# Kernel optimization log

Hardware: AMD Instinct MI355X
Metric: run time of the kernel (lower is better)

The kernel has to match this reference:

```python
import jax, jax.numpy as jnp
import numpy as np

VOCAB = 100
EMB = 256
HID = 256
B = 8
S = 2048


def setup_inputs() -> dict:
    key = jax.random.key(0)
    ks = jax.random.split(key, 12)
    s_e = 1.0 / np.sqrt(EMB)
    s_h = 1.0 / np.sqrt(HID)
    return {
        "x": jax.random.randint(ks[0], (B, S), 0, VOCAB),
        "embedding": jax.random.normal(ks[1], (VOCAB, EMB), jnp.float32),
        "w_ih": jax.random.uniform(ks[2], (3 * HID, EMB), jnp.float32, -s_e, s_e),
        "w_hh": jax.random.uniform(ks[3], (3 * HID, HID), jnp.float32, -s_h, s_h),
        "b_ih": jax.random.uniform(ks[4], (3 * HID,), jnp.float32, -s_h, s_h),
        "b_hh": jax.random.uniform(ks[5], (3 * HID,), jnp.float32, -s_h, s_h),
        "attn_w": jax.random.uniform(ks[6], (HID, HID), jnp.float32, -s_h, s_h),
        "attn_b": jax.random.uniform(ks[7], (HID,), jnp.float32, -s_h, s_h),
        "comb_w": jax.random.uniform(ks[8], (HID, 2 * HID), jnp.float32, -s_h, s_h),
        "comb_b": jax.random.uniform(ks[9], (HID,), jnp.float32, -s_h, s_h),
        "fc_w": jax.random.uniform(ks[10], (VOCAB, HID), jnp.float32, -s_h, s_h),
        "fc_b": jax.random.uniform(ks[11], (VOCAB,), jnp.float32, -s_h, s_h),
    }


def _gru(emb, w_ih, w_hh, b_ih, b_hh):
    # emb: [B, S, E]; PyTorch GRU gate order: r, z, n
    xg = jnp.einsum('bse,ge->bsg', emb, w_ih) + b_ih  # [B, S, 3H]
    h0 = jnp.zeros((emb.shape[0], HID), emb.dtype)

    def step(h, xg_t):
        hg = h @ w_hh.T + b_hh
        xr, xz, xn = jnp.split(xg_t, 3, axis=-1)
        hr, hz, hn = jnp.split(hg, 3, axis=-1)
        r = jax.nn.sigmoid(xr + hr)
        z = jax.nn.sigmoid(xz + hz)
        n = jnp.tanh(xn + r * hn)
        h_new = (1.0 - z) * n + z * h
        return h_new, h_new

    h_last, hs = jax.lax.scan(step, h0, jnp.swapaxes(xg, 0, 1))
    return jnp.swapaxes(hs, 0, 1), h_last  # [B,S,H], [B,H]


def reference(x, embedding, w_ih, w_hh, b_ih, b_hh, attn_w, attn_b, comb_w, comb_b, fc_w, fc_b):
    emb = embedding[x]  # [B, S, E]
    all_h, h_last = _gru(emb, w_ih, w_hh, b_ih, b_hh)
    keys = jnp.einsum('bsh,kh->bsk', all_h, attn_w) + attn_b  # [B,S,H]
    scores = jnp.einsum('bqh,bkh->bqk', all_h, keys)  # [B,S,S]
    seq = all_h.shape[1]
    causal = jnp.tril(jnp.ones((seq, seq), bool))
    scores = jnp.where(causal[None], scores, -jnp.inf)
    attn = jax.nn.softmax(scores, axis=-1)
    context = jnp.einsum('bqk,bkh->bqh', attn, all_h)  # [B,S,H]
    combined = jnp.concatenate([all_h, context], axis=-1)
    combined = jnp.tanh(jnp.einsum('bsd,hd->bsh', combined, comb_w) + comb_b)
    output = jnp.einsum('bsh,vh->bsv', combined, fc_w) + fc_b
    return output, h_last[None]  # hidden: [num_layers=1, B, H]
```

## Files before the change

kernel.cpp:

```cpp
#include <hip/hip_runtime.h>

#define SEQ  2048
#define NB   8
#define HD   256
#define G3   768
#define NV   100
#define KVB  32

typedef float f32x4 __attribute__((ext_vector_type(4)));
typedef int   i32x4 __attribute__((ext_vector_type(4)));
typedef short s16x8 __attribute__((ext_vector_type(8)));
typedef unsigned short u16x4 __attribute__((ext_vector_type(4)));

#define INV26 1.490116119384765625e-8f

__device__ __forceinline__ float rcp_fast(float x) {
  return __builtin_amdgcn_rcpf(x);
}
__device__ __forceinline__ float sigm(float x) {
  x = fminf(fmaxf(x, -30.f), 30.f);
  return rcp_fast(1.f + __expf(-x));
}
__device__ __forceinline__ float tanh_fast(float x) {
  x = fminf(fmaxf(x, -15.f), 15.f);
  float e = __expf(2.f * x);
  return (e - 1.f) * rcp_fast(e + 1.f);
}
__device__ __forceinline__ void cvt_hilo(float f, unsigned short& h, unsigned short& l) {
  unsigned u = __float_as_uint(f);
  h = (unsigned short)(u >> 16);
  float r = f - __uint_as_float(u & 0xffff0000u);
  l = (unsigned short)(__float_as_uint(r) >> 16);
}

__global__ __launch_bounds__(256) void build_table(
    const float* __restrict__ emb, const float* __restrict__ w_ih,
    const float* __restrict__ b_ih, float* __restrict__ table) {
  __shared__ float eL[256];
  __shared__ float wL[256][37];
  int v = blockIdx.x, tid = threadIdx.x;
  eL[tid] = emb[v * HD + tid];
  for (int gt = 0; gt < 3; ++gt) {
    float acc = b_ih[gt * 256 + tid];
    for (int e0 = 0; e0 < HD; e0 += 32) {
      __syncthreads();
      #pragma unroll
      for (int i = 0; i < 32; ++i) {
        int idx = tid + i * 256;
        int r = idx >> 5, c = idx & 31;
        wL[r][c] = w_ih[(size_t)(gt * 256 + r) * HD + e0 + c];
      }
      __syncthreads();
      #pragma unroll
      for (int c = 0; c < 32; ++c) acc += eL[e0 + c] * wL[tid][c];
    }
    table[((size_t)v * 256 + tid) * 4 + gt] = acc;
  }
}

__global__ void __launch_bounds__(512) gru_scan(
    const int* __restrict__ x, const float* __restrict__ w_hh,
    const float* __restrict__ b_hh, const float* __restrict__ table,
    float* __restrict__ all_h, float* __restrict__ h_last) {
  __shared__ __align__(16) signed char hpk[2][2 * 272];
  __shared__ int xs[SEQ];
  const int b = blockIdx.x;
  int tid = threadIdx.x;
  int lane = tid & 63, wv = tid >> 6;
  int ncol = lane & 15, quad = lane >> 4;
  int usel = quad & 1;
  int j = wv * 32 + usel * 16 + ncol;

  for (int i = tid; i < SEQ; i += 512) xs[i] = x[b * SEQ + i];
  for (int i = tid; i < 2 * 272; i += 512)
    hpk[0][i] = (i >= 272) ? (signed char)-128 : 0;

  i32x4 bw[2][3][4];
  float Cn2[2][3];
  #pragma unroll
  for (int u = 0; u < 2; ++u) {
    #pragma unroll
    for (int t3 = 0; t3 < 3; ++t3) {
      int row = t3 * 256 + wv * 32 + u * 16 + ncol;
      int sw = 0;
      #pragma unroll
      for (int c = 0; c < 4; ++c) {
        const float* p = w_hh + (size_t)row * HD + c * 64 + quad * 16;
        unsigned pw[4] = {0u, 0u, 0u, 0u};
        #pragma unroll
        for (int e = 0; e < 16; ++e) {
          int q = __float2int_rn(p[e] * 2048.f);
          q = max(-127, min(127, q));
          sw += q;
          pw[e >> 2] |= ((unsigned)(q & 255)) << ((e & 3) * 8);
        }
        bw[u][t3][c] = (i32x4){(int)pw[0], (int)pw[1], (int)pw[2], (int)pw[3]};
      }
      sw += __shfl_xor(sw, 16);
      sw += __shfl_xor(sw, 32);
      Cn2[u][t3] = b_hh[row] + 128.f * (float)sw * INV26;
    }
  }
  float Csel[3];
  #pragma unroll
  for (int t3 = 0; t3 < 3; ++t3) Csel[t3] = usel ? Cn2[1][t3] : Cn2[0][t3];

  float hreg = 0.f, hpend = 0.f;
  __syncthreads();
  float xr, xz, xn;
  {
    int v = xs[0];
    f32x4 xg = *(const f32x4*)&table[((size_t)v * 256 + j) * 4];
    xr = xg[0]; xz = xg[1]; xn = xg[2];
  }
  int a_base = (ncol & 1) * 272 + quad * 16;

  for (int t = 0; t < SEQ; ++t) {
    const signed char* cb = hpk[t & 1];
    i32x4 a[4];
    #pragma unroll
    for (int c = 0; c < 4; ++c)
      a[c] = *(const i32x4*)&cb[a_base + c * 64];
    if (t > 0 && quad < 2)
      all_h[((size_t)b * SEQ + (t - 1)) * HD + j] = hpend;
    int vnext = xs[(t + 1 < SEQ) ? t + 1 : t];
    f32x4 xgn = *(const f32x4*)&table[((size_t)vnext * 256 + j) * 4];
    float hg[3];
    #pragma unroll
    for (int t3 = 0; t3 < 3; ++t3) {
      i32x4 A0 = {0, 0, 0, 0}, A1 = {0, 0, 0, 0};
      #pragma unroll
      for (int c = 0; c < 4; ++c) {
        A0 = __builtin_amdgcn_mfma_i32_16x16x64_i8(a[c], bw[0][t3][c], A0, 0, 0, 0);
        A1 = __builtin_amdgcn_mfma_i32_16x16x64_i8(a[c], bw[1][t3][c], A1, 0, 0, 0);
      }
      int d0 = usel ? A1[0] : A0[0];
      int d1 = usel ? A1[1] : A0[1];
      hg[t3] = ((float)d0 * 256.f + (float)d1) * INV26 + Csel[t3];
    }
    float r = sigm(xr + hg[0]);
    float z = sigm(xz + hg[1]);
    float n = tanh_fast(xn + r * hg[2]);
    float h = (1.f - z) * n + z * hreg;
    hreg = h;
    hpend = h;
    int q = min(__float2int_rn(h * 32768.f), 32767);
    int lou = q & 255;
    int hi8 = (q - lou) >> 8;
    signed char* nx = hpk[(t + 1) & 1];
    if (quad < 2) {
      nx[j] = (signed char)hi8;
      nx[272 + j] = (signed char)(lou - 128);
    }
    xr = xgn[0]; xz = xgn[1]; xn = xgn[2];
    __syncthreads();
  }
  if (quad < 2) {
    all_h[((size_t)b * SEQ + (SEQ - 1)) * HD + j] = hpend;
    h_last[b * HD + j] = hreg;
  }
}

template<int ACT>
__global__ __launch_bounds__(256) void gemm_bias(
    const float* __restrict__ A, int lda,
    const float* __restrict__ W, const float* __restrict__ bias,
    float* __restrict__ C, int ldc, int N, int K) {
  __shared__ float As[128][36];
  __shared__ float Ws[64][36];
  int tid = threadIdx.x;
  int m0 = blockIdx.y * 128, n0 = blockIdx.x * 64;
  int ml = tid & 31, g = tid >> 5;
  float acc[4][8];
  #pragma unroll
  for (int i = 0; i < 4; ++i)
    #pragma unroll
    for (int jj = 0; jj < 8; ++jj) acc[i][jj] = 0.f;
  for (int k0 = 0; k0 < K; k0 += 32) {
    __syncthreads();
    #pragma unroll
    for (int i = 0; i < 4; ++i) {
      int idx = tid + i * 256;
      int r = idx >> 3, c4 = (idx & 7) * 4;
      *(f32x4*)&As[r][c4] = *(const f32x4*)&A[(size_t)(m0 + r) * lda + k0 + c4];
    }
    #pragma unroll
    for (int i = 0; i < 2; ++i) {
      int idx = tid + i * 256;
      int r = idx >> 3, c4 = (idx & 7) * 4;
      f32x4 wv = {0.f, 0.f, 0.f, 0.f};
      if (n0 + r < N) wv = *(const f32x4*)&W[(size_t)(n0 + r) * K + k0 + c4];
      *(f32x4*)&Ws[r][c4] = wv;
    }
    __syncthreads();
    #pragma unroll
    for (int k4 = 0; k4 < 32; k4 += 4) {
      f32x4 av[4], wv8[8];
      #pragma unroll
      for (int i = 0; i < 4; ++i) av[i] = *(const f32x4*)&As[ml + i * 32][k4];
      #pragma unroll
      for (int jj = 0; jj < 8; ++jj) wv8[jj] = *(const f32x4*)&Ws[g * 8 + jj][k4];
      #pragma unroll
      for (int kk = 0; kk < 4; ++kk)
        #pragma unroll
        for (int i = 0; i < 4; ++i)
          #pragma unroll
          for (int jj = 0; jj < 8; ++jj)
            acc[i][jj] += av[i][kk] * wv8[jj][kk];
    }
  }
  #pragma unroll
  for (int i = 0; i < 4; ++i) {
    int m = m0 + ml + i * 32;
    #pragma unroll
    for (int jj = 0; jj < 8; ++jj) {
      int n = n0 + g * 8 + jj;
      if (n < N) {
        float val = acc[i][jj] + bias[n];
        if (ACT) val = tanh_fast(val);
        C[(size_t)m * ldc + n] = val;
      }
    }
  }
}

__global__ __launch_bounds__(256) void gemm_bias_cat(
    const float* __restrict__ A1, const float* __restrict__ A2,
    const float* __restrict__ W, const float* __restrict__ bias,
    float* __restrict__ C) {
  __shared__ float As[128][36];
  __shared__ float Ws[64][36];
  const int K = 512;
  int tid = threadIdx.x;
  int m0 = blockIdx.y * 128, n0 = blockIdx.x * 64;
  int ml = tid & 31, g = tid >> 5;
  float acc[4][8];
  #pragma unroll
  for (int i = 0; i < 4; ++i)
    #pragma unroll
    for (int jj = 0; jj < 8; ++jj) acc[i][jj] = 0.f;
  for (int k0 = 0; k0 < K; k0 += 32) {
    const float* src = (k0 < 256) ? A1 : A2;
    int kb = (k0 < 256) ? k0 : k0 - 256;
    __syncthreads();
    #pragma unroll
    for (int i = 0; i < 4; ++i) {
      int idx = tid + i * 256;
      int r = idx >> 3, c4 = (idx & 7) * 4;
      *(f32x4*)&As[r][c4] = *(const f32x4*)&src[(size_t)(m0 + r) * 256 + kb + c4];
    }
    #pragma unroll
    for (int i = 0; i < 2; ++i) {
      int idx = tid + i * 256;
      int r = idx >> 3, c4 = (idx & 7) * 4;
      *(f32x4*)&Ws[r][c4] = *(const f32x4*)&W[(size_t)(n0 + r) * K + k0 + c4];
    }
    __syncthreads();
    #pragma unroll
    for (int k4 = 0; k4 < 32; k4 += 4) {
      f32x4 av[4], wv8[8];
      #pragma unroll
      for (int i = 0; i < 4; ++i) av[i] = *(const f32x4*)&As[ml + i * 32][k4];
      #pragma unroll
      for (int jj = 0; jj < 8; ++jj) wv8[jj] = *(const f32x4*)&Ws[g * 8 + jj][k4];
      #pragma unroll
      for (int kk = 0; kk < 4; ++kk)
        #pragma unroll
        for (int i = 0; i < 4; ++i)
          #pragma unroll
          for (int jj = 0; jj < 8; ++jj)
            acc[i][jj] += av[i][kk] * wv8[jj][kk];
    }
  }
  #pragma unroll
  for (int i = 0; i < 4; ++i) {
    int m = m0 + ml + i * 32;
    #pragma unroll
    for (int jj = 0; jj < 8; ++jj) {
      int n = n0 + g * 8 + jj;
      C[(size_t)m * 256 + n] = tanh_fast(acc[i][jj] + bias[n]);
    }
  }
}

__global__ __launch_bounds__(256, 1) void attention_kernel(
    const float* __restrict__ all_h, const float* __restrict__ keys,
    float* __restrict__ ctxg) {
  __shared__ __align__(16) unsigned short KH[2][8][4][140], KL[2][8][4][140];
  __shared__ __align__(16) unsigned short VH[16][524], VL[16][524];
  __shared__ __align__(16) unsigned short PB[4][2][520];
  const int b = blockIdx.y, qb = blockIdx.x;
  int tid = threadIdx.x, lane = tid & 63, wv = tid >> 6;
  int lm = lane & 15, kg = lane >> 4;
  const float* hb = all_h + (size_t)b * SEQ * HD;
  const float* kb = keys  + (size_t)b * SEQ * HD;
  const int q0 = qb * 64 + wv * 16;

  s16x8 Qh[8], Ql[8];
  {
    const float* qp = hb + (size_t)(q0 + lm) * HD;
    #pragma unroll
    for (int ch = 0; ch < 8; ++ch) {
      union { s16x8 v; unsigned short u[8]; } uh, ul;
      f32x4 a0 = *(const f32x4*)&qp[ch * 32 + kg * 8];
      f32x4 a1 = *(const f32x4*)&qp[ch * 32 + kg * 8 + 4];
      #pragma unroll
      for (int e = 0; e < 4; ++e) {
        cvt_hilo(a0[e], uh.u[e], ul.u[e]);
        cvt_hilo(a1[e], uh.u[4 + e], ul.u[4 + e]);
      }
      Qh[ch] = uh.v; Ql[ch] = ul.v;
    }
  }

  f32x4 co[16];
  #pragma unroll
  for (int ht = 0; ht < 16; ++ht) co[ht] = (f32x4){0.f, 0.f, 0.f, 0.f};
  float mo[4] = {-3e38f, -3e38f, -3e38f, -3e38f};
  float lr[4] = {0.f, 0.f, 0.f, 0.f};

  const int nkt = 2 * qb + 2;
  f32x4 kreg[8], vreg[8];
  {
    #pragma unroll
    for (int i = 0; i < 8; ++i) {
      int idx = tid + i * 256;
      int r = idx >> 6, c = idx & 63;
      kreg[i] = *(const f32x4*)&kb[(size_t)r * HD + c * 4];
      vreg[i] = *(const f32x4*)&hb[(size_t)r * HD + c * 4];
    }
  }
  for (int kt = 0; kt < nkt; ++kt) {
    __syncthreads();
    #pragma unroll
    for (int i = 0; i < 8; ++i) {
      int idx = tid + i * 256;
      int r = idx >> 6, c = idx & 63;
      f32x4 kv = kreg[i];
      f32x4 vv = vreg[i];
      u16x4 khv, klv;
      #pragma unroll
      for (int e = 0; e < 4; ++e) {
        unsigned short h16, l16;
        cvt_hilo(kv[e], h16, l16);
        khv[e] = h16; klv[e] = l16;
      }
      int off = (r & 15) * 8 + (c & 1) * 4;
      *(u16x4*)&KH[r >> 4][c >> 3][(c & 7) >> 1][off] = khv;
      *(u16x4*)&KL[r >> 4][c >> 3][(c & 7) >> 1][off] = klv;
      int kgv = r >> 3, ev = r & 7, ht = c >> 2;
      #pragma unroll
      for (int e = 0; e < 4; ++e) {
        unsigned short h16, l16;
        cvt_hilo(vv[e], h16, l16);
        int o = (kgv * 16 + (c & 3) * 4 + e) * 8 + ev;
        VH[ht][o] = h16; VL[ht][o] = l16;
      }
    }
    __syncthreads();
    if (kt + 1 < nkt) {
      int k1 = (kt + 1) * KVB;
      #pragma unroll
      for (int i = 0; i < 8; ++i) {
        int idx = tid + i * 256;
        int r = idx >> 6, c = idx & 63;
        kreg[i] = *(const f32x4*)&kb[(size_t)(k1 + r) * HD + c * 4];
        vreg[i] = *(const f32x4*)&hb[(size_t)(k1 + r) * HD + c * 4];
      }
    }
    int k0 = kt * KVB;

    float s[4][2];
    #pragma unroll
    for (int g = 0; g < 2; ++g) {
      f32x4 a0 = {0.f,0.f,0.f,0.f}, a1 = {0.f,0.f,0.f,0.f}, a2 = {0.f,0.f,0.f,0.f};
      #pragma unroll
      for (int ch = 0; ch < 8; ++ch) {
        s16x8 bh = *(const s16x8*)&KH[g][ch][kg][lm * 8];
        s16x8 bl = *(const s16x8*)&KL[g][ch][kg][lm * 8];
        a0 = __builtin_amdgcn_mfma_f32_16x16x32_bf16(Qh[ch], bh, a0, 0, 0, 0);
        a1 = __builtin_amdgcn_mfma_f32_16x16x32_bf16(Ql[ch], bh, a1, 0, 0, 0);
        a2 = __builtin_amdgcn_mfma_f32_16x16x32_bf16(Qh[ch], bl, a2, 0, 0, 0);
      }
      #pragma unroll
      for (int r = 0; r < 4; ++r) s[r][g] = a0[r] + a1[r] + a2[r];
    }
    float p[4][2], al[4];
    #pragma unroll
    for (int r = 0; r < 4; ++r) {
      int qrow = q0 + kg * 4 + r;
      int va = (k0 + lm) <= qrow, vb = (k0 + 16 + lm) <= qrow;
      float ta = va ? s[r][0] : -3e38f;
      float tb = vb ? s[r][1] : -3e38f;
      float t = fmaxf(ta, tb);
      t = fmaxf(t, __shfl_xor(t, 1));
      t = fmaxf(t, __shfl_xor(t, 2));
      t = fmaxf(t, __shfl_xor(t, 4));
      t = fmaxf(t, __shfl_xor(t, 8));
      float mn = fmaxf(mo[r], t);
      al[r] = __expf(mo[r] - mn);
      float pa = va ? __expf(s[r][0] - mn) : 0.f;
      float pb = vb ? __expf(s[r][1] - mn) : 0.f;
      p[r][0] = pa; p[r][1] = pb;
      float rs = pa + pb;
      rs += __shfl_xor(rs, 1);
      rs += __shfl_xor(rs, 2);
      rs += __shfl_xor(rs, 4);
      rs += __shfl_xor(rs, 8);
      lr[r] = lr[r] * al[r] + rs;
      mo[r] = mn;
    }
    #pragma unroll
    for (int r = 0; r < 4; ++r)
      #pragma unroll
      for (int g = 0; g < 2; ++g) {
        unsigned short ph, pl;
        cvt_hilo(p[r][g], ph, pl);
        int key = g * 16 + lm;
        int o = ((key >> 3) * 16 + kg * 4 + r) * 8 + (key & 7);
        PB[wv][0][o] = ph;
        PB[wv][1][o] = pl;
      }
    s16x8 pah = *(const s16x8*)&PB[wv][0][lane * 8];
    s16x8 pal = *(const s16x8*)&PB[wv][1][lane * 8];
    #pragma unroll
    for (int ht = 0; ht < 16; ++ht) {
      f32x4 c = co[ht];
      #pragma unroll
      for (int r = 0; r < 4; ++r) c[r] *= al[r];
      s16x8 vh = *(const s16x8*)&VH[ht][lane * 8];
      s16x8 vl = *(const s16x8*)&VL[ht][lane * 8];
      c = __builtin_amdgcn_mfma_f32_16x16x32_bf16(pah, vh, c, 0, 0, 0);
      c = __builtin_amdgcn_mfma_f32_16x16x32_bf16(pah, vl, c, 0, 0, 0);
      c = __builtin_amdgcn_mfma_f32_16x16x32_bf16(pal, vh, c, 0, 0, 0);
      co[ht] = c;
    }
  }
  float li[4];
  #pragma unroll
  for (int r = 0; r < 4; ++r) li[r] = rcp_fast(lr[r]);
  #pragma unroll
  for (int ht = 0; ht < 16; ++ht)
    #pragma unroll
    for (int r = 0; r < 4; ++r)
      ctxg[((size_t)b * SEQ + q0 + kg * 4 + r) * HD + ht * 16 + lm] = co[ht][r] * li[r];
}

extern "C" void kernel_launch(void* const* d_in, const int* in_sizes, int n_in,
                              void* d_out, int out_size, void* d_ws, size_t ws_size,
                              hipStream_t stream) {
  (void)in_sizes; (void)n_in; (void)out_size; (void)ws_size;
  const int*   x      = (const int*)  d_in[0];
  const float* emb    = (const float*)d_in[1];
  const float* w_ih   = (const float*)d_in[2];
  const float* w_hh   = (const float*)d_in[3];
  const float* b_ih   = (const float*)d_in[4];
  const float* b_hh   = (const float*)d_in[5];
  const float* attn_w = (const float*)d_in[6];
  const float* attn_b = (const float*)d_in[7];
  const float* comb_w = (const float*)d_in[8];
  const float* comb_b = (const float*)d_in[9];
  const float* fc_w   = (const float*)d_in[10];
  const float* fc_b   = (const float*)d_in[11];
  float* out = (float*)d_out;

  float* ws    = (float*)d_ws;
  float* table = ws;
  float* all_h = table + 102400;
  float* keys  = all_h + 4194304;
  float* ctx   = keys  + 4194304;
  float* hlast = out + (size_t)NB * SEQ * NV;

  build_table<<<100, 256, 0, stream>>>(emb, w_ih, b_ih, table);
  gru_scan<<<NB, 512, 0, stream>>>(x, w_hh, b_hh, table, all_h, hlast);
  gemm_bias<0><<<dim3(4, 128), 256, 0, stream>>>(all_h, 256, attn_w, attn_b, keys, 256, 256, 256);
  attention_kernel<<<dim3(32, 8), 256, 0, stream>>>(all_h, keys, ctx);
  gemm_bias_cat<<<dim3(4, 128), 256, 0, stream>>>(all_h, ctx, comb_w, comb_b, keys);
  gemm_bias<0><<<dim3(2, 128), 256, 0, stream>>>(keys, 256, fc_w, fc_b, out, 100, 100, 256);
}
```

Before: 2.104 ms.

## Prepack attention keys as bf16 hi/lo in MFMA layout inside keys GEMM

```diff
diff --git a/kernel.cpp b/kernel.cpp
--- a/kernel.cpp
+++ b/kernel.cpp
@@ -105,7 +105,7 @@
   #pragma unroll
   for (int t3 = 0; t3 < 3; ++t3) Csel[t3] = usel ? Cn2[1][t3] : Cn2[0][t3];
 
-  float hreg = 0.f, hpend = 0.f;
+  float hreg = 0.f;
   __syncthreads();
   float xr, xz, xn;
   {
@@ -121,10 +121,6 @@
     #pragma unroll
     for (int c = 0; c < 4; ++c)
       a[c] = *(const i32x4*)&cb[a_base + c * 64];
-    if (t > 0 && quad < 2)
-      all_h[((size_t)b * SEQ + (t - 1)) * HD + j] = hpend;
-    int vnext = xs[(t + 1 < SEQ) ? t + 1 : t];
-    f32x4 xgn = *(const f32x4*)&table[((size_t)vnext * 256 + j) * 4];
     float hg[3];
     #pragma unroll
     for (int t3 = 0; t3 < 3; ++t3) {
@@ -143,7 +139,6 @@
     float n = tanh_fast(xn + r * hg[2]);
     float h = (1.f - z) * n + z * hreg;
     hreg = h;
-    hpend = h;
     int q = min(__float2int_rn(h * 32768.f), 32767);
     int lou = q & 255;
     int hi8 = (q - lou) >> 8;
@@ -151,14 +146,14 @@
     if (quad < 2) {
       nx[j] = (signed char)hi8;
       nx[272 + j] = (signed char)(lou - 128);
-    }
-    xr = xgn[0]; xz = xgn[1]; xn = xgn[2];
-    __syncthreads();
-  }
-  if (quad < 2) {
-    all_h[((size_t)b * SEQ + (SEQ - 1)) * HD + j] = hpend;
-    h_last[b * HD + j] = hreg;
-  }
+      all_h[((size_t)b * SEQ + t) * HD + j] = h;
+    }
+    int v = xs[(t + 1 < SEQ) ? t + 1 : t];
+    f32x4 xg = *(const f32x4*)&table[((size_t)v * 256 + j) * 4];
+    xr = xg[0]; xz = xg[1]; xn = xg[2];
+    __syncthreads();
+  }
+  if (quad < 2) h_last[b * HD + j] = hreg;
 }
 
 template<int ACT>
@@ -224,6 +219,72 @@
   }
 }
 
+__global__ __launch_bounds__(256) void gemm_keys_pack(
+    const float* __restrict__ A,
+    const float* __restrict__ W, const float* __restrict__ bias,
+    unsigned short* __restrict__ KP) {
+  __shared__ float As[128][36];
+  __shared__ float Ws[64][36];
+  const int K = 256;
+  int tid = threadIdx.x;
+  int m0 = blockIdx.y * 128, n0 = blockIdx.x * 64;
+  int ml = tid & 31, gq = tid >> 5;
+  float acc[4][8];
+  #pragma unroll
+  for (int i = 0; i < 4; ++i)
+    #pragma unroll
+    for (int jj = 0; jj < 8; ++jj) acc[i][jj] = 0.f;
+  for (int k0 = 0; k0 < K; k0 += 32) {
+    __syncthreads();
+    #pragma unroll
+    for (int i = 0; i < 4; ++i) {
+      int idx = tid + i * 256;
+      int r = idx >> 3, c4 = (idx & 7) * 4;
+      *(f32x4*)&As[r][c4] = *(const f32x4*)&A[(size_t)(m0 + r) * HD + k0 + c4];
+    }
+    #pragma unroll
+    for (int i = 0; i < 2; ++i) {
+      int idx = tid + i * 256;
+      int r = idx >> 3, c4 = (idx & 7) * 4;
+      *(f32x4*)&Ws[r][c4] = *(const f32x4*)&W[(size_t)(n0 + r) * K + k0 + c4];
+    }
+    __syncthreads();
+    #pragma unroll
+    for (int k4 = 0; k4 < 32; k4 += 4) {
+      f32x4 av[4], wv8[8];
+      #pragma unroll
+      for (int i = 0; i < 4; ++i) av[i] = *(const f32x4*)&As[ml + i * 32][k4];
+      #pragma unroll
+      for (int jj = 0; jj < 8; ++jj) wv8[jj] = *(const f32x4*)&Ws[gq * 8 + jj][k4];
+      #pragma unroll
+      for (int kk = 0; kk < 4; ++kk)
+        #pragma unroll
+        for (int i = 0; i < 4; ++i)
+          #pragma unroll
+          for (int jj = 0; jj < 8; ++jj)
+            acc[i][jj] += av[i][kk] * wv8[jj][kk];
+    }
+  }
+  #pragma unroll
+  for (int i = 0; i < 4; ++i) {
+    int m = m0 + ml + i * 32;
+    int bb = m >> 11, key = m & 2047;
+    int kt = key >> 5, g = (key >> 4) & 1, lmk = key & 15;
+    int nb = n0 + gq * 8;
+    int ch = nb >> 5, kq = (nb >> 3) & 3;
+    size_t base = ((size_t)(bb * 64 + kt) * 32 + (g * 8 + ch) * 2) * 512
+                + (size_t)(lmk + kq * 16) * 8;
+    union { s16x8 v; unsigned short u[8]; } uh, ul;
+    #pragma unroll
+    for (int jj = 0; jj < 8; ++jj) {
+      float val = acc[i][jj] + bias[nb + jj];
+      cvt_hilo(val, uh.u[jj], ul.u[jj]);
+    }
+    *(s16x8*)&KP[base] = uh.v;
+    *(s16x8*)&KP[base + 512] = ul.v;
+  }
+}
+
 __global__ __launch_bounds__(256) void gemm_bias_cat(
     const float* __restrict__ A1, const float* __restrict__ A2,
     const float* __restrict__ W, const float* __restrict__ bias,
@@ -284,16 +345,16 @@
 }
 
 __global__ __launch_bounds__(256, 1) void attention_kernel(
-    const float* __restrict__ all_h, const float* __restrict__ keys,
+    const float* __restrict__ all_h, const unsigned short* __restrict__ kp,
     float* __restrict__ ctxg) {
-  __shared__ __align__(16) unsigned short KH[2][8][4][140], KL[2][8][4][140];
+  __shared__ __align__(16) unsigned short KU[32 * 512];
   __shared__ __align__(16) unsigned short VH[16][524], VL[16][524];
   __shared__ __align__(16) unsigned short PB[4][2][520];
   const int b = blockIdx.y, qb = blockIdx.x;
   int tid = threadIdx.x, lane = tid & 63, wv = tid >> 6;
   int lm = lane & 15, kg = lane >> 4;
   const float* hb = all_h + (size_t)b * SEQ * HD;
-  const float* kb = keys  + (size_t)b * SEQ * HD;
+  const unsigned short* kpb = kp + (size_t)b * 64 * 16384;
   const int q0 = qb * 64 + wv * 16;
 
   s16x8 Qh[8], Ql[8];
@@ -320,13 +381,18 @@
   float lr[4] = {0.f, 0.f, 0.f, 0.f};
 
   const int nkt = 2 * qb + 2;
-  f32x4 kreg[8], vreg[8];
+  s16x8 kp8[8];
+  f32x4 vreg[8];
   {
     #pragma unroll
     for (int i = 0; i < 8; ++i) {
+      int up = wv + i * 4;
+      kp8[i] = *(const s16x8*)&kpb[(size_t)up * 512 + lane * 8];
+    }
+    #pragma unroll
+    for (int i = 0; i < 8; ++i) {
       int idx = tid + i * 256;
       int r = idx >> 6, c = idx & 63;
-      kreg[i] = *(const f32x4*)&kb[(size_t)r * HD + c * 4];
       vreg[i] = *(const f32x4*)&hb[(size_t)r * HD + c * 4];
     }
   }
@@ -334,20 +400,14 @@
     __syncthreads();
     #pragma unroll
     for (int i = 0; i < 8; ++i) {
+      int up = wv + i * 4;
+      *(s16x8*)&KU[up * 512 + lane * 8] = kp8[i];
+    }
+    #pragma unroll
+    for (int i = 0; i < 8; ++i) {
       int idx = tid + i * 256;
       int r = idx >> 6, c = idx & 63;
-      f32x4 kv = kreg[i];
       f32x4 vv = vreg[i];
-      u16x4 khv, klv;
-      #pragma unroll
-      for (int e = 0; e < 4; ++e) {
-        unsigned short h16, l16;
-        cvt_hilo(kv[e], h16, l16);
-        khv[e] = h16; klv[e] = l16;
-      }
-      int off = (r & 15) * 8 + (c & 1) * 4;
-      *(u16x4*)&KH[r >> 4][c >> 3][(c & 7) >> 1][off] = khv;
-      *(u16x4*)&KL[r >> 4][c >> 3][(c & 7) >> 1][off] = klv;
       int kgv = r >> 3, ev = r & 7, ht = c >> 2;
       #pragma unroll
       for (int e = 0; e < 4; ++e) {
@@ -359,12 +419,17 @@
     }
     __syncthreads();
     if (kt + 1 < nkt) {
+      const unsigned short* tb = kpb + (size_t)(kt + 1) * 16384;
+      #pragma unroll
+      for (int i = 0; i < 8; ++i) {
+        int up = wv + i * 4;
+        kp8[i] = *(const s16x8*)&tb[(size_t)up * 512 + lane * 8];
+      }
       int k1 = (kt + 1) * KVB;
       #pragma unroll
       for (int i = 0; i < 8; ++i) {
         int idx = tid + i * 256;
         int r = idx >> 6, c = idx & 63;
-        kreg[i] = *(const f32x4*)&kb[(size_t)(k1 + r) * HD + c * 4];
         vreg[i] = *(const f32x4*)&hb[(size_t)(k1 + r) * HD + c * 4];
       }
     }
@@ -376,8 +441,9 @@
       f32x4 a0 = {0.f,0.f,0.f,0.f}, a1 = {0.f,0.f,0.f,0.f}, a2 = {0.f,0.f,0.f,0.f};
       #pragma unroll
       for (int ch = 0; ch < 8; ++ch) {
-        s16x8 bh = *(const s16x8*)&KH[g][ch][kg][lm * 8];
-        s16x8 bl = *(const s16x8*)&KL[g][ch][kg][lm * 8];
+        const unsigned short* ub = &KU[((g * 8 + ch) * 2) * 512 + lane * 8];
+        s16x8 bh = *(const s16x8*)ub;
+        s16x8 bl = *(const s16x8*)(ub + 512);
         a0 = __builtin_amdgcn_mfma_f32_16x16x32_bf16(Qh[ch], bh, a0, 0, 0, 0);
         a1 = __builtin_amdgcn_mfma_f32_16x16x32_bf16(Ql[ch], bh, a1, 0, 0, 0);
         a2 = __builtin_amdgcn_mfma_f32_16x16x32_bf16(Qh[ch], bl, a2, 0, 0, 0);
@@ -467,14 +533,15 @@
   float* ws    = (float*)d_ws;
   float* table = ws;
   float* all_h = table + 102400;
-  float* keys  = all_h + 4194304;
-  float* ctx   = keys  + 4194304;
+  float* keysb = all_h + 4194304;
+  float* ctx   = keysb + 4194304;
   float* hlast = out + (size_t)NB * SEQ * NV;
+  unsigned short* kpack = (unsigned short*)keysb;
 
   build_table<<<100, 256, 0, stream>>>(emb, w_ih, b_ih, table);
   gru_scan<<<NB, 512, 0, stream>>>(x, w_hh, b_hh, table, all_h, hlast);
-  gemm_bias<0><<<dim3(4, 128), 256, 0, stream>>>(all_h, 256, attn_w, attn_b, keys, 256, 256, 256);
-  attention_kernel<<<dim3(32, 8), 256, 0, stream>>>(all_h, keys, ctx);
-  gemm_bias_cat<<<dim3(4, 128), 256, 0, stream>>>(all_h, ctx, comb_w, comb_b, keys);
-  gemm_bias<0><<<dim3(2, 128), 256, 0, stream>>>(keys, 256, fc_w, fc_b, out, 100, 100, 256);
-}
+  gemm_keys_pack<<<dim3(4, 128), 256, 0, stream>>>(all_h, attn_w, attn_b, kpack);
+  attention_kernel<<<dim3(32, 8), 256, 0, stream>>>(all_h, kpack, ctx);
+  gemm_bias_cat<<<dim3(4, 128), 256, 0, stream>>>(all_h, ctx, comb_w, comb_b, keysb);
+  gemm_bias<0><<<dim3(2, 128), 256, 0, stream>>>(keysb, 256, fc_w, fc_b, out, 100, 100, 256);
+}
```

New measurement: 1.880 ms. -10.7%, faster.
